# Kernel tuning notes

Hardware: AMD Instinct MI355X
Metric: run time of the kernel (lower is better)

Reference implementation:

```python
import jax, jax.numpy as jnp
import numpy as np

V, E, Hd, B, S = 50000, 256, 256, 128, 128  # vocab, embed, hidden, batch, seq


def setup_inputs() -> dict:
    key = jax.random.key(0)
    ks = jax.random.split(key, 16)
    std = 1.0 / np.sqrt(Hd)

    def u(k, shape, lim):
        return jax.random.uniform(k, shape, jnp.float32, -lim, lim)

    emb_table = jax.random.normal(ks[0], (V, E), jnp.float32)
    emb_table = emb_table.at[0].set(0.0)  # padding_idx=0

    inp = {
        'batch_size': B,
        'input_Q': jax.random.randint(ks[1], (S, B), 0, V),
        'input_C': jax.random.randint(ks[2], (S, B), 0, V),
        'input_C2': jax.random.randint(ks[3], (S, B), 0, V),
        'hidden_Q': jnp.zeros((2, B, Hd), jnp.float32),
        'cell_Q': jnp.zeros((2, B, Hd), jnp.float32),
        'hidden_C': jnp.zeros((2, B, Hd), jnp.float32),
        'cell_C': jnp.zeros((2, B, Hd), jnp.float32),
        'hidden_C2': jnp.zeros((2, B, Hd), jnp.float32),
        'cell_C2': jnp.zeros((2, B, Hd), jnp.float32),
        'emb_table': emb_table,
        'Wih_f': u(ks[4], (4 * Hd, E), std), 'Whh_f': u(ks[5], (4 * Hd, Hd), std),
        'bih_f': u(ks[6], (4 * Hd,), std), 'bhh_f': u(ks[7], (4 * Hd,), std),
        'Wih_b': u(ks[8], (4 * Hd, E), std), 'Whh_b': u(ks[9], (4 * Hd, Hd), std),
        'bih_b': u(ks[10], (4 * Hd,), std), 'bhh_b': u(ks[11], (4 * Hd,), std),
        'S1_W': u(ks[12], (2 * Hd, 2 * Hd), 0.1),  # init_weights: uniform(-0.1, 0.1)
        'S1_b': u(ks[13], (2 * Hd,), 1.0 / np.sqrt(2 * Hd)),
    }
    return inp


def _lstm_dir(xs, h0, c0, Wih, Whh, b):
    # xs: [S,B,E]; single direction LSTM, torch gate order i,f,g,o
    def step(carry, xt):
        h, c = carry
        g = xt @ Wih.T + h @ Whh.T + b  # [B,4H]
        i, f, gg, o = jnp.split(g, 4, axis=-1)
        c = jax.nn.sigmoid(f) * c + jax.nn.sigmoid(i) * jnp.tanh(gg)
        h = jax.nn.sigmoid(o) * jnp.tanh(c)
        return (h, c), h
    _, ys = jax.lax.scan(step, (h0, c0), xs)
    return ys  # [S,B,H]


def _bilstm(x, h0, c0, Wih_f, Whh_f, bih_f, bhh_f, Wih_b, Whh_b, bih_b, bhh_b):
    # x: [B,S,E] -> [B,S,2H]
    xs = jnp.swapaxes(x, 0, 1)
    yf = _lstm_dir(xs, h0[0], c0[0], Wih_f, Whh_f, bih_f + bhh_f)
    yb = _lstm_dir(xs[::-1], h0[1], c0[1], Wih_b, Whh_b, bih_b + bhh_b)[::-1]
    return jnp.swapaxes(jnp.concatenate([yf, yb], axis=-1), 0, 1)


def _attention(Q, C0, S1_W, S1_b):
    # Batched version of the per-sample loop: Q,C0 [B,S,2H]
    C = jnp.tanh(C0 @ S1_W.T + S1_b)                      # tanh(S1(C0))
    Hm = jnp.einsum('bsd,btd->bst', Q, C)                 # Q @ C.T
    AQ = jax.nn.softmax(Hm, axis=-1)                      # softmax over rows (torch dim=1 for 2D)
    AC = jax.nn.softmax(jnp.swapaxes(Hm, 1, 2), axis=-1)  # softmax(H.T)
    MQ = jnp.einsum('bst,btd->bsd', AQ, Q)
    MC = jnp.einsum('bst,btd->bsd', AC, MQ)
    b = Q.shape[0]
    return MQ.reshape(b, -1), MC.reshape(b, -1)


def reference(batch_size, input_Q, input_C, input_C2, hidden_Q, cell_Q,
              hidden_C, cell_C, hidden_C2, cell_C2, emb_table,
              Wih_f, Whh_f, bih_f, bhh_f, Wih_b, Whh_b, bih_b, bhh_b,
              S1_W, S1_b):
    lstm_w = (Wih_f, Whh_f, bih_f, bhh_f, Wih_b, Whh_b, bih_b, bhh_b)
    # forward() transposes [S,B] -> [B,S] before embedding
    q = emb_table[input_Q.T]
    c = emb_table[input_C.T]
    c2 = emb_table[input_C2.T]
    out_q = _bilstm(q, hidden_Q, cell_Q, *lstm_w)
    out_c = _bilstm(c, hidden_C, cell_C, *lstm_w)
    out_c2 = _bilstm(c2, hidden_C2, cell_C2, *lstm_w)
    attn_Q1, attn_C = _attention(out_q, out_c, S1_W, S1_b)
    attn_Q2, attn_C2 = _attention(out_q, out_c2, S1_W, S1_b)
    return (attn_Q1, attn_C, attn_Q2, attn_C2)
```

## Files before the change

kernel.cpp:

```cpp
#include <hip/hip_runtime.h>
#include <math.h>

namespace {

constexpr int S = 128;
constexpr int B = 128;
constexpr int E = 256;
constexpr int H = 256;

typedef unsigned short u16;
typedef __attribute__((ext_vector_type(8))) short short8v;
typedef __attribute__((ext_vector_type(4))) float f32x4;

__device__ __forceinline__ float sigmoidf(float x) { return 1.0f / (1.0f + expf(-x)); }
__device__ __forceinline__ u16 bf16rnd(float x) {
  unsigned u = __float_as_uint(x);
  return (u16)((u + 0x7FFFu + ((u >> 16) & 1u)) >> 16);
}
__device__ __forceinline__ float bf2f(u16 v) { return __uint_as_float(((unsigned)v) << 16); }
__device__ __forceinline__ void split2(float x, u16& h, u16& l) {
  h = bf16rnd(x);
  l = bf16rnd(x - bf2f(h));
}
__device__ __forceinline__ int gcol_of(int c) {
  return ((c >> 4) & 3) * 256 + ((c & 15) + ((c >> 6) << 4));
}


__global__ void split_pair(const float* __restrict__ src, u16* __restrict__ h,
                           u16* __restrict__ l, long n) {
  long i = (long)blockIdx.x * 256 + threadIdx.x;
  if (i < n) split2(src[i], h[i], l[i]);
}

__global__ void split_w_int(const float* __restrict__ W, u16* __restrict__ h,
                            u16* __restrict__ l) {
  int i = blockIdx.x * 256 + threadIdx.x;
  int c = i >> 8, k = i & 255;
  split2(W[gcol_of(c) * 256 + k], h[i], l[i]);
}

__global__ void make_bint(const float* __restrict__ bih, const float* __restrict__ bhh,
                          float* __restrict__ bint) {
  int c = blockIdx.x * 256 + threadIdx.x;
  int g = gcol_of(c);
  bint[c] = bih[g] + bhh[g];
}

__global__ void init_hc(const float* hQ, const float* cQ, const float* hC, const float* cC,
                        const float* hC2, const float* cC2,
                        u16* hH, u16* hL, float* cst) {
  int i = blockIdx.x * 256 + threadIdx.x;
  if (i >= 6 * B * H) return;
  int z = i / (B * H);
  int rem = i - z * (B * H);
  int input = z >> 1, dir = z & 1;
  const float* hs = input == 0 ? hQ : (input == 1 ? hC : hC2);
  const float* cs = input == 0 ? cQ : (input == 1 ? cC : cC2);
  split2(hs[dir * B * H + rem], hH[i], hL[i]);
  cst[i] = cs[dir * B * H + rem];
}

__global__ void zero_gen(int* gen) {
  if (threadIdx.x < 6) gen[threadIdx.x * 256] = 0;
}


#define MFMA_PROLOG                                        \
  const int tid = threadIdx.x;                             \
  const int wave = tid >> 6, lane = tid & 63;              \
  const int wr = wave >> 1, wc = wave & 1;                 \
  const int lrow = lane & 15, lk = lane >> 4;              \
  f32x4 acc[4][4];

#define MFMA_ZERO_ACC                                      \
  _Pragma("unroll") for (int a_ = 0; a_ < 4; ++a_)         \
  _Pragma("unroll") for (int b_ = 0; b_ < 4; ++b_)         \
      acc[a_][b_] = (f32x4){0.f, 0.f, 0.f, 0.f};

#define MFMA_INNER                                                             \
  __syncthreads();                                                             \
  short8v ah[4], al[4];                                                        \
  _Pragma("unroll") for (int mt = 0; mt < 4; ++mt) {                           \
    int r_ = wr * 64 + mt * 16 + lrow;                                         \
    ah[mt] = *(const short8v*)&Ah[r_ * 40 + lk * 8];                           \
    al[mt] = *(const short8v*)&Al[r_ * 40 + lk * 8];                           \
  }                                                                            \
  _Pragma("unroll") for (int nt = 0; nt < 4; ++nt) {                           \
    int c_ = wc * 64 + nt * 16 + lrow;                                         \
    short8v bh = *(const short8v*)&Bh[c_ * 40 + lk * 8];                       \
    short8v bl = *(const short8v*)&Bl[c_ * 40 + lk * 8];                       \
    _Pragma("unroll") for (int mt = 0; mt < 4; ++mt) {                         \
      acc[mt][nt] = __builtin_amdgcn_mfma_f32_16x16x32_bf16(ah[mt], bh, acc[mt][nt], 0, 0, 0); \
      acc[mt][nt] = __builtin_amdgcn_mfma_f32_16x16x32_bf16(ah[mt], bl, acc[mt][nt], 0, 0, 0); \
      acc[mt][nt] = __builtin_amdgcn_mfma_f32_16x16x32_bf16(al[mt], bh, acc[mt][nt], 0, 0, 0); \
    }                                                                          \
  }

__global__ __launch_bounds__(256) void proj_mfma(
    const int* __restrict__ idxQ, const int* __restrict__ idxC, const int* __restrict__ idxC2,
    const u16* __restrict__ embH, const u16* __restrict__ embL,
    const u16* __restrict__ wHf, const u16* __restrict__ wLf,
    const u16* __restrict__ wHb, const u16* __restrict__ wLb,
    const float* __restrict__ bintf, const float* __restrict__ bintb,
    float* __restrict__ gi, int phase)
{
  const int z = blockIdx.z, input = z >> 1, dir = z & 1;
  const int n0 = blockIdx.x * 128;
  const int tl = blockIdx.y;
  const int tb = (dir == 0) ? phase * 64 + tl : (64 - phase * 64) + tl;
  const int* idx = input == 0 ? idxQ : (input == 1 ? idxC : idxC2);
  const u16* wH = dir ? wHb : wHf;
  const u16* wL = dir ? wLb : wLf;
  const float* bint = dir ? bintb : bintf;

  __shared__ __align__(16) short Ah[128 * 40], Al[128 * 40], Bh[128 * 40], Bl[128 * 40];
  __shared__ int tok[128];
  MFMA_PROLOG
  if (tid < 128) tok[tid] = idx[tb * B + tid];
  MFMA_ZERO_ACC

  for (int kb = 0; kb < E; kb += 32) {
    __syncthreads();
#pragma unroll
    for (int i = 0; i < 2; ++i) {
      int e = i * 256 + tid;
      int r = e >> 2, kg = e & 3;
      long abase = (long)tok[r] * E + kb + kg * 8;
      *(short8v*)&Ah[r * 40 + kg * 8] = *(const short8v*)(embH + abase);
      *(short8v*)&Al[r * 40 + kg * 8] = *(const short8v*)(embL + abase);
      long bbase = (long)(n0 + r) * E + kb + kg * 8;
      *(short8v*)&Bh[r * 40 + kg * 8] = *(const short8v*)(wH + bbase);
      *(short8v*)&Bl[r * 40 + kg * 8] = *(const short8v*)(wL + bbase);
    }
    MFMA_INNER
  }

  float* gp = gi + ((long)z * 64 + tl) * 1024 * 128;
#pragma unroll
  for (int mt = 0; mt < 4; ++mt)
#pragma unroll
    for (int nt = 0; nt < 4; ++nt) {
      int c = n0 + wc * 64 + nt * 16 + lrow;
      float bv = bint[c];
      f32x4 v = acc[mt][nt];
      v.x += bv; v.y += bv; v.z += bv; v.w += bv;
      int rowb = wr * 64 + mt * 16 + lk * 4;
      *(f32x4*)&gp[(long)c * 128 + rowb] = v;
    }
}

__global__ __launch_bounds__(256) void lstm_persist(
    const u16* __restrict__ whHf, const u16* __restrict__ whLf,
    const u16* __restrict__ whHb, const u16* __restrict__ whLb,
    const float* __restrict__ gi,
    u16* __restrict__ hH, u16* __restrict__ hL, float* __restrict__ cst,
    u16* __restrict__ out3h, u16* __restrict__ out3l,
    int* __restrict__ gen, int phase)
{
  const int bx = blockIdx.x;
  const int z = bx >> 4, nb = bx & 15;
  const int input = z >> 1, dir = z & 1;
  const int n0c = nb * 64;
  const int tid = threadIdx.x;
  const int wave = tid >> 6, lane = tid & 63;
  const int lrow = lane & 15, lk = lane >> 4;
  const int wr = wave;
  const u16* wHp = dir ? whHb : whHf;
  const u16* wLp = dir ? whLb : whLf;

  __shared__ __align__(16) short WlH[64 * 264], WlL[64 * 264];

#pragma unroll
  for (int i = 0; i < 8; ++i) {
    int e = i * 256 + tid;
    int c = e >> 5, kc = e & 31;
    *(short8v*)&WlH[c * 264 + kc * 8] = *(const short8v*)(wHp + (long)(n0c + c) * 256 + kc * 8);
    *(short8v*)&WlL[c * 264 + kc * 8] = *(const short8v*)(wLp + (long)(n0c + c) * 256 + kc * 8);
  }
  __syncthreads();

  const long HS = (long)6 * B * H;
  const long zb = (long)z * B * H;
  const int u = nb * 16 + lrow;
  int* genz = gen + z * 256;
  u16* o3h = out3h + (long)input * B * S * 512;
  u16* o3l = out3l + (long)input * B * S * 512;

  for (int tl = 0; tl < 64; ++tl) {
    const int t_global = phase * 64 + tl;
    const int t_eff = dir ? (S - 1 - t_global) : t_global;
    const int local = (dir == 0) ? tl : 63 - tl;
    const int par = t_global & 1;

    f32x4 gv[2][4];
    {
      const float* gp = gi + ((long)z * 64 + local) * 1024 * 128;
#pragma unroll
      for (int mt = 0; mt < 2; ++mt)
#pragma unroll
        for (int nt = 0; nt < 4; ++nt) {
          int c = n0c + nt * 16 + lrow;
          int rowb = wr * 32 + mt * 16 + lk * 4;
          gv[mt][nt] = *(const f32x4*)&gp[(long)c * 128 + rowb];
        }
    }

    if (tl > 0) {
      if (tid == 0) {
        const int target = 16 * tl;
        while (__hip_atomic_load(genz, __ATOMIC_ACQUIRE, __HIP_MEMORY_SCOPE_AGENT) < target) {
          __builtin_amdgcn_s_sleep(2);
        }
      }
      __syncthreads();
    }

    const u16* hrH = hH + (long)par * HS + zb;
    const u16* hrL = hL + (long)par * HS + zb;

    f32x4 acc[2][4];
#pragma unroll
    for (int mt = 0; mt < 2; ++mt)
#pragma unroll
      for (int nt = 0; nt < 4; ++nt) acc[mt][nt] = gv[mt][nt];

#pragma unroll
    for (int kb = 0; kb < 8; ++kb) {
      short8v ah[2], al[2];
#pragma unroll
      for (int mt = 0; mt < 2; ++mt) {
        long ho = (long)(wr * 32 + mt * 16 + lrow) * 256 + kb * 32 + lk * 8;
        ah[mt] = *(const short8v*)(hrH + ho);
        al[mt] = *(const short8v*)(hrL + ho);
      }
#pragma unroll
      for (int nt = 0; nt < 4; ++nt) {
        int c = nt * 16 + lrow;
        short8v bh = *(const short8v*)&WlH[c * 264 + kb * 32 + lk * 8];
        short8v bl = *(const short8v*)&WlL[c * 264 + kb * 32 + lk * 8];
#pragma unroll
        for (int mt = 0; mt < 2; ++mt) {
          acc[mt][nt] = __builtin_amdgcn_mfma_f32_16x16x32_bf16(ah[mt], bh, acc[mt][nt], 0, 0, 0);
          acc[mt][nt] = __builtin_amdgcn_mfma_f32_16x16x32_bf16(ah[mt], bl, acc[mt][nt], 0, 0, 0);
          acc[mt][nt] = __builtin_amdgcn_mfma_f32_16x16x32_bf16(al[mt], bh, acc[mt][nt], 0, 0, 0);
        }
      }
    }

    float* cz = cst + zb;
    u16* hwH = hH + (long)(par ^ 1) * HS + zb;
    u16* hwL = hL + (long)(par ^ 1) * HS + zb;
#pragma unroll
    for (int mt = 0; mt < 2; ++mt)
#pragma unroll
      for (int rg = 0; rg < 4; ++rg) {
        int row = wr * 32 + mt * 16 + lk * 4 + rg;
        float ig = sigmoidf(acc[mt][0][rg]);
        float fg = sigmoidf(acc[mt][1][rg]);
        float gg = tanhf(acc[mt][2][rg]);
        float og = sigmoidf(acc[mt][3][rg]);
        long ci = (long)row * H + u;
        float cn = fg * cz[ci] + ig * gg;
        cz[ci] = cn;
        float hn = og * tanhf(cn);
        u16 hh, hl;
        split2(hn, hh, hl);
        hwH[ci] = hh;
        hwL[ci] = hl;
        long oi = ((long)row * S + t_eff) * 512 + dir * 256 + u;
        o3h[oi] = hh;
        o3l[oi] = hl;
      }

    asm volatile("s_waitcnt vmcnt(0)" ::: "memory");
    __syncthreads();
    if (tid == 0) {
      __hip_atomic_fetch_add(genz, 1, __ATOMIC_RELEASE, __HIP_MEMORY_SCOPE_AGENT);
    }
  }
}

__global__ __launch_bounds__(256) void ct_mfma(
    const u16* __restrict__ aH, const u16* __restrict__ aL,
    const u16* __restrict__ s1H, const u16* __restrict__ s1L,
    const float* __restrict__ s1b,
    u16* __restrict__ ctH, u16* __restrict__ ctL)
{
  const int n0 = blockIdx.x * 128, m0 = blockIdx.y * 128;
  __shared__ __align__(16) short Ah[128 * 40], Al[128 * 40], Bh[128 * 40], Bl[128 * 40];
  MFMA_PROLOG
  MFMA_ZERO_ACC

  for (int kb = 0; kb < 512; kb += 32) {
    __syncthreads();
#pragma unroll
    for (int i = 0; i < 2; ++i) {
      int e = i * 256 + tid;
      int r = e >> 2, kg = e & 3;
      long abase = (long)(m0 + r) * 512 + kb + kg * 8;
      *(short8v*)&Ah[r * 40 + kg * 8] = *(const short8v*)(aH + abase);
      *(short8v*)&Al[r * 40 + kg * 8] = *(const short8v*)(aL + abase);
      long bbase = (long)(n0 + r) * 512 + kb + kg * 8;
      *(short8v*)&Bh[r * 40 + kg * 8] = *(const short8v*)(s1H + bbase);
      *(short8v*)&Bl[r * 40 + kg * 8] = *(const short8v*)(s1L + bbase);
    }
    MFMA_INNER
  }

#pragma unroll
  for (int mt = 0; mt < 4; ++mt)
#pragma unroll
    for (int nt = 0; nt < 4; ++nt) {
      int c = n0 + wc * 64 + nt * 16 + lrow;
      float bv = s1b[c];
#pragma unroll
      for (int rg = 0; rg < 4; ++rg) {
        long m = m0 + wr * 64 + mt * 16 + lk * 4 + rg;
        u16 hh, ll;
        split2(tanhf(acc[mt][nt][rg] + bv), hh, ll);
        ctH[m * 512 + c] = hh;
        ctL[m * 512 + c] = ll;
      }
    }
}

__global__ __launch_bounds__(256) void hm_mfma(
    const u16* __restrict__ qH, const u16* __restrict__ qL,
    const u16* __restrict__ ctH, const u16* __restrict__ ctL,
    float* __restrict__ Hm)
{
  const int bb = blockIdx.x;
  const u16* aH = qH + (long)bb * S * 512;
  const u16* aL = qL + (long)bb * S * 512;
  const u16* bH = ctH + (long)bb * S * 512;
  const u16* bL = ctL + (long)bb * S * 512;
  __shared__ __align__(16) short Ah[128 * 40], Al[128 * 40], Bh[128 * 40], Bl[128 * 40];
  MFMA_PROLOG
  MFMA_ZERO_ACC

  for (int kb = 0; kb < 512; kb += 32) {
    __syncthreads();
#pragma unroll
    for (int i = 0; i < 2; ++i) {
      int e = i * 256 + tid;
      int r = e >> 2, kg = e & 3;
      long base = (long)r * 512 + kb + kg * 8;
      *(short8v*)&Ah[r * 40 + kg * 8] = *(const short8v*)(aH + base);
      *(short8v*)&Al[r * 40 + kg * 8] = *(const short8v*)(aL + base);
      *(short8v*)&Bh[r * 40 + kg * 8] = *(const short8v*)(bH + base);
      *(short8v*)&Bl[r * 40 + kg * 8] = *(const short8v*)(bL + base);
    }
    MFMA_INNER
  }

  float* out = Hm + (long)bb * S * S;
#pragma unroll
  for (int mt = 0; mt < 4; ++mt)
#pragma unroll
    for (int nt = 0; nt < 4; ++nt) {
      int c = wc * 64 + nt * 16 + lrow;
#pragma unroll
      for (int rg = 0; rg < 4; ++rg) {
        int m = wr * 64 + mt * 16 + lk * 4 + rg;
        out[(long)m * S + c] = acc[mt][nt][rg];
      }
    }
}

__global__ void transpose_qt(const u16* __restrict__ o3h, const u16* __restrict__ o3l,
                             u16* __restrict__ qth, u16* __restrict__ qtl) {
  const int b = blockIdx.z;
  const int c0 = blockIdx.x * 64, t0 = blockIdx.y * 64;
  __shared__ u16 tile[64][72];
  const int tid = threadIdx.x;
  for (int pl = 0; pl < 2; ++pl) {
    const u16* src = (pl ? o3l : o3h) + (long)b * S * 512;
    u16* dst = (pl ? qtl : qth) + (long)b * 512 * 128;
    __syncthreads();
#pragma unroll
    for (int i = 0; i < 2; ++i) {
      int e = i * 256 + tid;
      int r = e >> 3, sg = e & 7;
      *(short8v*)&tile[r][sg * 8] = *(const short8v*)(src + (long)(t0 + r) * 512 + c0 + sg * 8);
    }
    __syncthreads();
#pragma unroll
    for (int i = 0; i < 2; ++i) {
      int e = i * 256 + tid;
      int c = e >> 3, sg = e & 7;
      short8v v;
#pragma unroll
      for (int j = 0; j < 8; ++j) v[j] = tile[sg * 8 + j][c];
      *(short8v*)(dst + (long)(c0 + c) * 128 + t0 + sg * 8) = v;
    }
  }
}

template <bool WRITE_T>
__global__ __launch_bounds__(256) void pq_mfma(
    const u16* __restrict__ pH, const u16* __restrict__ pL,
    const u16* __restrict__ btH, const u16* __restrict__ btL,
    float* __restrict__ Cout, u16* __restrict__ tH, u16* __restrict__ tL)
{
  const int bb = blockIdx.z, n0 = blockIdx.x * 128;
  const u16* aHp = pH + (long)bb * 128 * 128;
  const u16* aLp = pL + (long)bb * 128 * 128;
  const u16* bHp = btH + ((long)bb * 512 + n0) * 128;
  const u16* bLp = btL + ((long)bb * 512 + n0) * 128;
  __shared__ __align__(16) short Ah[128 * 40], Al[128 * 40], Bh[128 * 40], Bl[128 * 40];
  MFMA_PROLOG
  MFMA_ZERO_ACC

  for (int kb = 0; kb < 128; kb += 32) {
    __syncthreads();
#pragma unroll
    for (int i = 0; i < 2; ++i) {
      int e = i * 256 + tid;
      int r = e >> 2, kg = e & 3;
      long base = (long)r * 128 + kb + kg * 8;
      *(short8v*)&Ah[r * 40 + kg * 8] = *(const short8v*)(aHp + base);
      *(short8v*)&Al[r * 40 + kg * 8] = *(const short8v*)(aLp + base);
      *(short8v*)&Bh[r * 40 + kg * 8] = *(const short8v*)(bHp + base);
      *(short8v*)&Bl[r * 40 + kg * 8] = *(const short8v*)(bLp + base);
    }
    MFMA_INNER
  }

  float* co = Cout + (long)bb * 128 * 512;
#pragma unroll
  for (int mt = 0; mt < 4; ++mt)
#pragma unroll
    for (int nt = 0; nt < 4; ++nt) {
      int c = n0 + wc * 64 + nt * 16 + lrow;
#pragma unroll
      for (int rg = 0; rg < 4; ++rg) {
        int m = wr * 64 + mt * 16 + lk * 4 + rg;
        float v = acc[mt][nt][rg];
        co[(long)m * 512 + c] = v;
        if (WRITE_T) {
          u16 hh, ll;
          split2(v, hh, ll);
          tH[((long)bb * 512 + c) * 128 + m] = hh;
          tL[((long)bb * 512 + c) * 128 + m] = ll;
        }
      }
    }
}

__global__ void softmax_row_bf(const float* __restrict__ Hm, u16* __restrict__ ph,
                               u16* __restrict__ pl) {
  const int row = blockIdx.x;
  const float* p = Hm + (long)row * S;
  const int l = threadIdx.x;
  float v0 = p[l], v1 = p[l + 64];
  float m = fmaxf(v0, v1);
#pragma unroll
  for (int o = 32; o > 0; o >>= 1) m = fmaxf(m, __shfl_xor(m, o));
  float e0 = expf(v0 - m), e1 = expf(v1 - m);
  float s = e0 + e1;
#pragma unroll
  for (int o = 32; o > 0; o >>= 1) s += __shfl_xor(s, o);
  float inv = 1.0f / s;
  u16 hh, ll;
  split2(e0 * inv, hh, ll);
  ph[(long)row * S + l] = hh; pl[(long)row * S + l] = ll;
  split2(e1 * inv, hh, ll);
  ph[(long)row * S + l + 64] = hh; pl[(long)row * S + l + 64] = ll;
}

__global__ void softmax_colT_bf(const float* __restrict__ Hm, u16* __restrict__ ph,
                                u16* __restrict__ pl) {
  const int b = blockIdx.x >> 7;
  const int col = blockIdx.x & 127;
  const float* p = Hm + (long)b * S * S + col;
  const int l = threadIdx.x;
  float v0 = p[(long)l * S], v1 = p[(long)(l + 64) * S];
  float m = fmaxf(v0, v1);
#pragma unroll
  for (int o = 32; o > 0; o >>= 1) m = fmaxf(m, __shfl_xor(m, o));
  float e0 = expf(v0 - m), e1 = expf(v1 - m);
  float s = e0 + e1;
#pragma unroll
  for (int o = 32; o > 0; o >>= 1) s += __shfl_xor(s, o);
  float inv = 1.0f / s;
  long q = ((long)b * S + col) * S;
  u16 hh, ll;
  split2(e0 * inv, hh, ll);
  ph[q + l] = hh; pl[q + l] = ll;
  split2(e1 * inv, hh, ll);
  ph[q + l + 64] = hh; pl[q + l + 64] = ll;
}

__global__ void softmax_row(const float* __restrict__ Hm, float* __restrict__ A) {
  const int row = blockIdx.x;
  const float* p = Hm + (long)row * S;
  const int l = threadIdx.x;
  float v0 = p[l], v1 = p[l + 64];
  float m = fmaxf(v0, v1);
#pragma unroll
  for (int o = 32; o > 0; o >>= 1) m = fmaxf(m, __shfl_xor(m, o));
  float e0 = expf(v0 - m), e1 = expf(v1 - m);
  float s = e0 + e1;
#pragma unroll
  for (int o = 32; o > 0; o >>= 1) s += __shfl_xor(s, o);
  float inv = 1.0f / s;
  float* q = A + (long)row * S;
  q[l] = e0 * inv; q[l + 64] = e1 * inv;
}

__global__ void softmax_colT(const float* __restrict__ Hm, float* __restrict__ A) {
  const int b = blockIdx.x >> 7;
  const int col = blockIdx.x & 127;
  const float* p = Hm + (long)b * S * S + col;
  const int l = threadIdx.x;
  float v0 = p[(long)l * S], v1 = p[(long)(l + 64) * S];
  float m = fmaxf(v0, v1);
#pragma unroll
  for (int o = 32; o > 0; o >>= 1) m = fmaxf(m, __shfl_xor(m, o));
  float e0 = expf(v0 - m), e1 = expf(v1 - m);
  float s = e0 + e1;
#pragma unroll
  for (int o = 32; o > 0; o >>= 1) s += __shfl_xor(s, o);
  float inv = 1.0f / s;
  float* q = A + ((long)b * S + col) * S;
  q[l] = e0 * inv; q[l + 64] = e1 * inv;
}


__global__ void init_state(const float* hQ, const float* cQ,
                           const float* hC, const float* cC,
                           const float* hC2, const float* cC2,
                           float* h0, float* c0) {
  int i = blockIdx.x * 256 + threadIdx.x;
  if (i >= 6 * B * H) return;
  int z = i / (B * H);
  int rem = i - z * (B * H);
  int input = z >> 1, dir = z & 1;
  const float* hs = input == 0 ? hQ : (input == 1 ? hC : hC2);
  const float* cs = input == 0 ? cQ : (input == 1 ? cC : cC2);
  h0[i] = hs[dir * B * H + rem];
  c0[i] = cs[dir * B * H + rem];
}

__global__ __launch_bounds__(256) void lstm_step(
    const int* __restrict__ idxQ, const int* __restrict__ idxC, const int* __restrict__ idxC2,
    const float* __restrict__ emb,
    const float* __restrict__ Wih_f, const float* __restrict__ Whh_f,
    const float* __restrict__ bih_f, const float* __restrict__ bhh_f,
    const float* __restrict__ Wih_b, const float* __restrict__ Whh_b,
    const float* __restrict__ bih_b, const float* __restrict__ bhh_b,
    const float* __restrict__ hread, float* __restrict__ hwrite,
    float* __restrict__ cstate, float* __restrict__ out3, int t)
{
  const int z = blockIdx.z;
  const int input = z >> 1, dir = z & 1;
  const int u0 = blockIdx.x * 16;
  const int b0 = blockIdx.y * 64;
  const int t_eff = dir ? (S - 1 - t) : t;
  const int* idx = input == 0 ? idxQ : (input == 1 ? idxC : idxC2);
  const float* Wih = dir ? Wih_b : Wih_f;
  const float* Whh = dir ? Whh_b : Whh_f;
  const float* bih = dir ? bih_b : bih_f;
  const float* bhh = dir ? bhh_b : bhh_f;

  __shared__ float Alds[64][68];
  __shared__ float Wl[64][68];
  __shared__ int tok[64];

  const int tid = threadIdx.x;
  if (tid < 64) tok[tid] = idx[t_eff * B + b0 + tid];

  const int uu = tid & 15;
  const int rg = tid >> 4;
  const int u = u0 + uu;

  float acc[4][4];
#pragma unroll
  for (int ri = 0; ri < 4; ++ri)
#pragma unroll
    for (int g = 0; g < 4; ++g)
      acc[ri][g] = bih[g * 256 + u] + bhh[g * 256 + u];

  for (int kc = 0; kc < 8; ++kc) {
    __syncthreads();
    if (kc < 4) {
      const int kb = kc * 64;
#pragma unroll
      for (int i = 0; i < 16; ++i) {
        int e = i * 256 + tid;
        int kk = e & 63, r = e >> 6;
        Alds[r][kk] = emb[(long)tok[r] * E + kb + kk];
      }
    } else {
      const int kb = (kc - 4) * 64;
      const float* hs = hread + ((long)z * B + b0) * H + kb;
#pragma unroll
      for (int i = 0; i < 16; ++i) {
        int e = i * 256 + tid;
        int kk = e & 63, r = e >> 6;
        Alds[r][kk] = hs[r * H + kk];
      }
    }
    {
      const float* Wsrc = (kc < 4) ? Wih : Whh;
      const int kb = (kc & 3) * 64;
#pragma unroll
      for (int i = 0; i < 16; ++i) {
        int e = i * 256 + tid;
        int kk = e & 63, c = e >> 6;
        int gcol = (c >> 4) * 256 + u0 + (c & 15);
        Wl[c][kk] = Wsrc[(long)gcol * H + kb + kk];
      }
    }
    __syncthreads();
#pragma unroll
    for (int k4 = 0; k4 < 64; k4 += 4) {
      float4 a[4], w[4];
#pragma unroll
      for (int ri = 0; ri < 4; ++ri) a[ri] = *(const float4*)&Alds[rg * 4 + ri][k4];
#pragma unroll
      for (int g = 0; g < 4; ++g) w[g] = *(const float4*)&Wl[g * 16 + uu][k4];
#pragma unroll
      for (int ri = 0; ri < 4; ++ri)
#pragma unroll
        for (int g = 0; g < 4; ++g)
          acc[ri][g] += a[ri].x * w[g].x + a[ri].y * w[g].y
                      + a[ri].z * w[g].z + a[ri].w * w[g].w;
    }
  }

  float* cs = cstate + (long)z * B * H;
  float* hw = hwrite + (long)z * B * H;
  float* op = out3 + (long)input * B * S * 2 * H;
#pragma unroll
  for (int ri = 0; ri < 4; ++ri) {
    int b = b0 + rg * 4 + ri;
    float ig = sigmoidf(acc[ri][0]);
    float fg = sigmoidf(acc[ri][1]);
    float gg = tanhf(acc[ri][2]);
    float og = sigmoidf(acc[ri][3]);
    float cn = fg * cs[b * H + u] + ig * gg;
    float hn = og * tanhf(cn);
    cs[b * H + u] = cn;
    hw[b * H + u] = hn;
    op[((long)b * S + t_eff) * (2 * H) + dir * H + u] = hn;
  }
}

template <bool TANH>
__global__ __launch_bounds__(256) void gemm_nt(
    const float* __restrict__ A, const float* __restrict__ B_,
    const float* __restrict__ bias, float* __restrict__ C,
    int lda, int ldb, int ldc, int K, long sA, long sB, long sC)
{
  A += blockIdx.z * sA; B_ += blockIdx.z * sB; C += blockIdx.z * sC;
  const int n0 = blockIdx.x * 64, m0 = blockIdx.y * 64;
  __shared__ float Alds[64][68], Blds[64][68];
  const int tid = threadIdx.x, uu = tid & 15, rg = tid >> 4;
  float acc[4][4] = {};
  for (int kb = 0; kb < K; kb += 64) {
    __syncthreads();
#pragma unroll
    for (int i = 0; i < 16; ++i) {
      int e = i * 256 + tid;
      int kk = e & 63, r = e >> 6;
      Alds[r][kk] = A[(long)(m0 + r) * lda + kb + kk];
      Blds[r][kk] = B_[(long)(n0 + r) * ldb + kb + kk];
    }
    __syncthreads();
#pragma unroll
    for (int k4 = 0; k4 < 64; k4 += 4) {
      float4 a[4], w[4];
#pragma unroll
      for (int ri = 0; ri < 4; ++ri) a[ri] = *(const float4*)&Alds[rg * 4 + ri][k4];
#pragma unroll
      for (int ci = 0; ci < 4; ++ci) w[ci] = *(const float4*)&Blds[ci * 16 + uu][k4];
#pragma unroll
      for (int ri = 0; ri < 4; ++ri)
#pragma unroll
        for (int ci = 0; ci < 4; ++ci)
          acc[ri][ci] += a[ri].x * w[ci].x + a[ri].y * w[ci].y
                       + a[ri].z * w[ci].z + a[ri].w * w[ci].w;
    }
  }
#pragma unroll
  for (int ri = 0; ri < 4; ++ri) {
    int m = m0 + rg * 4 + ri;
#pragma unroll
    for (int ci = 0; ci < 4; ++ci) {
      int n = n0 + ci * 16 + uu;
      float v = acc[ri][ci];
      if (bias) v += bias[n];
      if (TANH) v = tanhf(v);
      C[(long)m * ldc + n] = v;
    }
  }
}

__global__ __launch_bounds__(256) void gemm_nn(
    const float* __restrict__ A, const float* __restrict__ B_,
    float* __restrict__ C,
    int lda, int ldb, int ldc, int K, long sA, long sB, long sC)
{
  A += blockIdx.z * sA; B_ += blockIdx.z * sB; C += blockIdx.z * sC;
  const int n0 = blockIdx.x * 64, m0 = blockIdx.y * 64;
  __shared__ float Alds[64][68];
  __shared__ float Blds[64][68];
  const int tid = threadIdx.x, uu = tid & 15, rg = tid >> 4;
  float acc[4][4] = {};
  for (int kb = 0; kb < K; kb += 64) {
    __syncthreads();
#pragma unroll
    for (int i = 0; i < 16; ++i) {
      int e = i * 256 + tid;
      int kk = e & 63, r = e >> 6;
      Alds[r][kk] = A[(long)(m0 + r) * lda + kb + kk];
      Blds[r][kk] = B_[(long)(kb + r) * ldb + n0 + kk];
    }
    __syncthreads();
#pragma unroll
    for (int kk = 0; kk < 64; ++kk) {
      float4 w = *(const float4*)&Blds[kk][uu * 4];
      float a0 = Alds[rg * 4 + 0][kk], a1 = Alds[rg * 4 + 1][kk];
      float a2 = Alds[rg * 4 + 2][kk], a3 = Alds[rg * 4 + 3][kk];
      acc[0][0] += a0 * w.x; acc[0][1] += a0 * w.y; acc[0][2] += a0 * w.z; acc[0][3] += a0 * w.w;
      acc[1][0] += a1 * w.x; acc[1][1] += a1 * w.y; acc[1][2] += a1 * w.z; acc[1][3] += a1 * w.w;
      acc[2][0] += a2 * w.x; acc[2][1] += a2 * w.y; acc[2][2] += a2 * w.z; acc[2][3] += a2 * w.w;
      acc[3][0] += a3 * w.x; acc[3][1] += a3 * w.y; acc[3][2] += a3 * w.z; acc[3][3] += a3 * w.w;
    }
  }
#pragma unroll
  for (int ri = 0; ri < 4; ++ri) {
    int m = m0 + rg * 4 + ri;
    float4 v = make_float4(acc[ri][0], acc[ri][1], acc[ri][2], acc[ri][3]);
    *(float4*)&C[(long)m * ldc + n0 + uu * 4] = v;
  }
}

}

extern "C" void kernel_launch(void* const* d_in, const int* in_sizes, int n_in,
                              void* d_out, int out_size, void* d_ws, size_t ws_size,
                              hipStream_t stream) {
  const int* idxQ    = (const int*)d_in[1];
  const int* idxC    = (const int*)d_in[2];
  const int* idxC2   = (const int*)d_in[3];
  const float* hQ    = (const float*)d_in[4];
  const float* cQ    = (const float*)d_in[5];
  const float* hC    = (const float*)d_in[6];
  const float* cC    = (const float*)d_in[7];
  const float* hC2   = (const float*)d_in[8];
  const float* cC2   = (const float*)d_in[9];
  const float* emb   = (const float*)d_in[10];
  const float* Wih_f = (const float*)d_in[11];
  const float* Whh_f = (const float*)d_in[12];
  const float* bih_f = (const float*)d_in[13];
  const float* bhh_f = (const float*)d_in[14];
  const float* Wih_b = (const float*)d_in[15];
  const float* Whh_b = (const float*)d_in[16];
  const float* bih_b = (const float*)d_in[17];
  const float* bhh_b = (const float*)d_in[18];
  const float* S1W   = (const float*)d_in[19];
  const float* S1b   = (const float*)d_in[20];
  float* out = (float*)d_out;

  const long V = 50000;
  const long OUT1 = (long)B * S * 2 * H;

  size_t off = 0;
  auto alloc = [&](size_t bytes) { size_t o = off; off += (bytes + 255) & ~(size_t)255; return o; };
  const size_t o_gi   = alloc((size_t)6 * 64 * 1024 * 128 * 4);
  const size_t o_o3h  = alloc((size_t)3 * B * S * 512 * 2);
  const size_t o_o3l  = alloc((size_t)3 * B * S * 512 * 2);
  const size_t o_embH = alloc((size_t)V * E * 2);
  const size_t o_embL = alloc((size_t)V * E * 2);
  const size_t o_wihHf = alloc(1024 * 256 * 2), o_wihLf = alloc(1024 * 256 * 2);
  const size_t o_wihHb = alloc(1024 * 256 * 2), o_wihLb = alloc(1024 * 256 * 2);
  const size_t o_whhHf = alloc(1024 * 256 * 2), o_whhLf = alloc(1024 * 256 * 2);
  const size_t o_whhHb = alloc(1024 * 256 * 2), o_whhLb = alloc(1024 * 256 * 2);
  const size_t o_s1H  = alloc(512 * 512 * 2), o_s1L = alloc(512 * 512 * 2);
  const size_t o_bintf = alloc(1024 * 4), o_bintb = alloc(1024 * 4);
  const size_t o_hH   = alloc((size_t)2 * 6 * B * H * 2);
  const size_t o_hL   = alloc((size_t)2 * 6 * B * H * 2);
  const size_t o_cst  = alloc((size_t)6 * B * H * 4);
  const size_t o_gen  = alloc(6 * 256 * 4);
  const size_t need_fast = off;

  if (ws_size >= need_fast) {
    char* base = (char*)d_ws;
    float* gi = (float*)(base + o_gi);
    u16* o3h = (u16*)(base + o_o3h);
    u16* o3l = (u16*)(base + o_o3l);
    u16* embH = (u16*)(base + o_embH);
    u16* embL = (u16*)(base + o_embL);
    u16* wihHf = (u16*)(base + o_wihHf); u16* wihLf = (u16*)(base + o_wihLf);
    u16* wihHb = (u16*)(base + o_wihHb); u16* wihLb = (u16*)(base + o_wihLb);
    u16* whhHf = (u16*)(base + o_whhHf); u16* whhLf = (u16*)(base + o_whhLf);
    u16* whhHb = (u16*)(base + o_whhHb); u16* whhLb = (u16*)(base + o_whhLb);
    u16* s1H = (u16*)(base + o_s1H); u16* s1L = (u16*)(base + o_s1L);
    float* bintf = (float*)(base + o_bintf);
    float* bintb = (float*)(base + o_bintb);
    u16* hH = (u16*)(base + o_hH);
    u16* hL = (u16*)(base + o_hL);
    float* cst = (float*)(base + o_cst);
    int* gen = (int*)(base + o_gen);
    char* gib = base + o_gi;
    u16* ctH = (u16*)gib;
    u16* ctL = (u16*)(gib + 16777216);
    float* Hm = (float*)(gib + 2 * 16777216);
    u16* Ph  = (u16*)(gib + 2 * 16777216 + 8388608);
    u16* Pl  = (u16*)(gib + 2 * 16777216 + 8388608 + 4194304);
    u16* QtH = (u16*)(gib + 2 * 16777216 + 8388608 + 2 * 4194304);
    u16* QtL = (u16*)(gib + 3 * 16777216 + 8388608 + 2 * 4194304);
    u16* MQtH = (u16*)(gib + 4 * 16777216 + 8388608 + 2 * 4194304);
    u16* MQtL = (u16*)(gib + 5 * 16777216 + 8388608 + 2 * 4194304);

    split_pair<<<(int)((V * E + 255) / 256), 256, 0, stream>>>(emb, embH, embL, V * E);
    split_w_int<<<1024, 256, 0, stream>>>(Wih_f, wihHf, wihLf);
    split_w_int<<<1024, 256, 0, stream>>>(Wih_b, wihHb, wihLb);
    split_w_int<<<1024, 256, 0, stream>>>(Whh_f, whhHf, whhLf);
    split_w_int<<<1024, 256, 0, stream>>>(Whh_b, whhHb, whhLb);
    split_pair<<<1024, 256, 0, stream>>>(S1W, s1H, s1L, 512 * 512);
    make_bint<<<4, 256, 0, stream>>>(bih_f, bhh_f, bintf);
    make_bint<<<4, 256, 0, stream>>>(bih_b, bhh_b, bintb);
    init_hc<<<(6 * B * H + 255) / 256, 256, 0, stream>>>(hQ, cQ, hC, cC, hC2, cC2, hH, hL, cst);

    for (int phase = 0; phase < 2; ++phase) {
      proj_mfma<<<dim3(8, 64, 6), 256, 0, stream>>>(
          idxQ, idxC, idxC2, embH, embL,
          wihHf, wihLf, wihHb, wihLb, bintf, bintb, gi, phase);
      zero_gen<<<1, 64, 0, stream>>>(gen);
      {
        const u16* a0 = whhHf; const u16* a1 = whhLf;
        const u16* a2 = whhHb; const u16* a3 = whhLb;
        const float* a4 = gi; u16* a5 = hH; u16* a6 = hL;
        float* a7 = cst; u16* a8 = o3h; u16* a9 = o3l;
        int* a10 = gen; int a11 = phase;
        void* kargs[] = {(void*)&a0, (void*)&a1, (void*)&a2, (void*)&a3,
                         (void*)&a4, (void*)&a5, (void*)&a6, (void*)&a7,
                         (void*)&a8, (void*)&a9, (void*)&a10, (void*)&a11};
        hipLaunchCooperativeKernel((const void*)lstm_persist, dim3(96), dim3(256),
                                   kargs, 0, stream);
      }
    }

    transpose_qt<<<dim3(8, 2, 128), 256, 0, stream>>>(o3h, o3l, QtH, QtL);
    for (int p = 0; p < 2; ++p) {
      const u16* aH = o3h + (size_t)(1 + p) * B * S * 512;
      const u16* aL = o3l + (size_t)(1 + p) * B * S * 512;
      ct_mfma<<<dim3(4, 128), 256, 0, stream>>>(aH, aL, s1H, s1L, S1b, ctH, ctL);
      hm_mfma<<<128, 256, 0, stream>>>(o3h, o3l, ctH, ctL, Hm);
      softmax_row_bf<<<B * S, 64, 0, stream>>>(Hm, Ph, Pl);
      float* MQ = out + (long)(2 * p) * OUT1;
      pq_mfma<true><<<dim3(4, 1, 128), 256, 0, stream>>>(
          Ph, Pl, QtH, QtL, MQ, MQtH, MQtL);
      softmax_colT_bf<<<B * S, 64, 0, stream>>>(Hm, Ph, Pl);
      float* MC = out + (long)(2 * p + 1) * OUT1;
      pq_mfma<false><<<dim3(4, 1, 128), 256, 0, stream>>>(
          Ph, Pl, MQtH, MQtL, MC, nullptr, nullptr);
    }
    return;
  }

  const long ST = (long)6 * B * H;
  float* ws    = (float*)d_ws;
  float* out3  = ws;
  float* hbuf0 = out3 + 3 * OUT1;
  float* hbuf1 = hbuf0 + ST;
  float* cbuf  = hbuf1 + ST;
  float* Ct    = cbuf + ST;
  float* Hm    = Ct + OUT1;
  float* Ab    = Hm + (long)B * S * S;

  init_state<<<(6 * B * H + 255) / 256, 256, 0, stream>>>(hQ, cQ, hC, cC, hC2, cC2, hbuf0, cbuf);

  for (int t = 0; t < S; ++t) {
    float* hr = (t & 1) ? hbuf1 : hbuf0;
    float* hw = (t & 1) ? hbuf0 : hbuf1;
    lstm_step<<<dim3(16, 2, 6), 256, 0, stream>>>(
        idxQ, idxC, idxC2, emb,
        Wih_f, Whh_f, bih_f, bhh_f, Wih_b, Whh_b, bih_b, bhh_b,
        hr, hw, cbuf, out3, t);
  }

  for (int p = 0; p < 2; ++p) {
    const float* Q  = out3;
    const float* C0 = out3 + (long)(1 + p) * OUT1;
    gemm_nt<true><<<dim3(8, 256, 1), 256, 0, stream>>>(
        C0, S1W, S1b, Ct, 512, 512, 512, 512, 0, 0, 0);
    gemm_nt<false><<<dim3(2, 2, B), 256, 0, stream>>>(
        Q, Ct, nullptr, Hm, 512, 512, 128, 512,
        (long)S * 512, (long)S * 512, (long)S * S);
    softmax_row<<<B * S, 64, 0, stream>>>(Hm, Ab);
    float* MQ = out + (long)(2 * p) * OUT1;
    gemm_nn<<<dim3(8, 2, B), 256, 0, stream>>>(
        Ab, Q, MQ, 128, 512, 512, 128,
        (long)S * S, (long)S * 512, (long)S * 512);
    softmax_colT<<<B * S, 64, 0, stream>>>(Hm, Ab);
    float* MC = out + (long)(2 * p + 1) * OUT1;
    gemm_nn<<<dim3(8, 2, B), 256, 0, stream>>>(
        Ab, MQ, MC, 128, 512, 512, 128,
        (long)S * S, (long)S * 512, (long)S * 512);
  }
}
```

Measured before the change: 2.498 ms.

## Fuse input projection into persistent LSTM kernel and keep cell state in registers

Removes the separate proj_mfma input-projection GEMM and its large gi buffer. Each persistent block now keeps both W_ih and W_hh slices in LDS, gathers embedding rows per timestep and computes the input projection before waiting on the generation barrier, so that work overlaps the wait for other blocks' h. The cell state is held in registers instead of global memory, and the two phases become one cooperative launch of 128 blocks (96 active). The cost is doubled LDS per block and gather loads from the embedding table on the recurrent critical path.

```diff
diff --git a/kernel.cpp b/kernel.cpp
--- a/kernel.cpp
+++ b/kernel.cpp
@@ -97,148 +97,102 @@
     }                                                                          \
   }
 
-__global__ __launch_bounds__(256) void proj_mfma(
+__global__ __launch_bounds__(256) void lstm_fused(
     const int* __restrict__ idxQ, const int* __restrict__ idxC, const int* __restrict__ idxC2,
     const u16* __restrict__ embH, const u16* __restrict__ embL,
-    const u16* __restrict__ wHf, const u16* __restrict__ wLf,
-    const u16* __restrict__ wHb, const u16* __restrict__ wLb,
+    const u16* __restrict__ wihHf, const u16* __restrict__ wihLf,
+    const u16* __restrict__ wihHb, const u16* __restrict__ wihLb,
+    const u16* __restrict__ whhHf, const u16* __restrict__ whhLf,
+    const u16* __restrict__ whhHb, const u16* __restrict__ whhLb,
     const float* __restrict__ bintf, const float* __restrict__ bintb,
-    float* __restrict__ gi, int phase)
-{
-  const int z = blockIdx.z, input = z >> 1, dir = z & 1;
-  const int n0 = blockIdx.x * 128;
-  const int tl = blockIdx.y;
-  const int tb = (dir == 0) ? phase * 64 + tl : (64 - phase * 64) + tl;
-  const int* idx = input == 0 ? idxQ : (input == 1 ? idxC : idxC2);
-  const u16* wH = dir ? wHb : wHf;
-  const u16* wL = dir ? wLb : wLf;
-  const float* bint = dir ? bintb : bintf;
-
-  __shared__ __align__(16) short Ah[128 * 40], Al[128 * 40], Bh[128 * 40], Bl[128 * 40];
-  __shared__ int tok[128];
-  MFMA_PROLOG
-  if (tid < 128) tok[tid] = idx[tb * B + tid];
-  MFMA_ZERO_ACC
-
-  for (int kb = 0; kb < E; kb += 32) {
-    __syncthreads();
-#pragma unroll
-    for (int i = 0; i < 2; ++i) {
-      int e = i * 256 + tid;
-      int r = e >> 2, kg = e & 3;
-      long abase = (long)tok[r] * E + kb + kg * 8;
-      *(short8v*)&Ah[r * 40 + kg * 8] = *(const short8v*)(embH + abase);
-      *(short8v*)&Al[r * 40 + kg * 8] = *(const short8v*)(embL + abase);
-      long bbase = (long)(n0 + r) * E + kb + kg * 8;
-      *(short8v*)&Bh[r * 40 + kg * 8] = *(const short8v*)(wH + bbase);
-      *(short8v*)&Bl[r * 40 + kg * 8] = *(const short8v*)(wL + bbase);
-    }
-    MFMA_INNER
-  }
-
-  float* gp = gi + ((long)z * 64 + tl) * 1024 * 128;
-#pragma unroll
-  for (int mt = 0; mt < 4; ++mt)
-#pragma unroll
-    for (int nt = 0; nt < 4; ++nt) {
-      int c = n0 + wc * 64 + nt * 16 + lrow;
-      float bv = bint[c];
-      f32x4 v = acc[mt][nt];
-      v.x += bv; v.y += bv; v.z += bv; v.w += bv;
-      int rowb = wr * 64 + mt * 16 + lk * 4;
-      *(f32x4*)&gp[(long)c * 128 + rowb] = v;
-    }
-}
-
-__global__ __launch_bounds__(256) void lstm_persist(
-    const u16* __restrict__ whHf, const u16* __restrict__ whLf,
-    const u16* __restrict__ whHb, const u16* __restrict__ whLb,
-    const float* __restrict__ gi,
-    u16* __restrict__ hH, u16* __restrict__ hL, float* __restrict__ cst,
+    u16* __restrict__ hH, u16* __restrict__ hL, const float* __restrict__ cst0,
     u16* __restrict__ out3h, u16* __restrict__ out3l,
-    int* __restrict__ gen, int phase)
+    int* __restrict__ gen)
 {
   const int bx = blockIdx.x;
-  const int z = bx >> 4, nb = bx & 15;
+  const int z = bx & 7;
+  if (z >= 6) return;
+  const int nb = bx >> 3;
   const int input = z >> 1, dir = z & 1;
   const int n0c = nb * 64;
   const int tid = threadIdx.x;
   const int wave = tid >> 6, lane = tid & 63;
   const int lrow = lane & 15, lk = lane >> 4;
   const int wr = wave;
-  const u16* wHp = dir ? whHb : whHf;
-  const u16* wLp = dir ? whLb : whLf;
-
-  __shared__ __align__(16) short WlH[64 * 264], WlL[64 * 264];
+  const int* idx = input == 0 ? idxQ : (input == 1 ? idxC : idxC2);
+  const u16* wiHp = dir ? wihHb : wihHf;
+  const u16* wiLp = dir ? wihLb : wihLf;
+  const u16* whHp = dir ? whhHb : whhHf;
+  const u16* whLp = dir ? whhLb : whhLf;
+  const float* bint = dir ? bintb : bintf;
+
+  __shared__ __align__(16) short WiH[64 * 264], WiL[64 * 264];
+  __shared__ __align__(16) short WhH[64 * 264], WhL[64 * 264];
+  __shared__ int tok[128];
 
 #pragma unroll
   for (int i = 0; i < 8; ++i) {
     int e = i * 256 + tid;
     int c = e >> 5, kc = e & 31;
-    *(short8v*)&WlH[c * 264 + kc * 8] = *(const short8v*)(wHp + (long)(n0c + c) * 256 + kc * 8);
-    *(short8v*)&WlL[c * 264 + kc * 8] = *(const short8v*)(wLp + (long)(n0c + c) * 256 + kc * 8);
-  }
-  __syncthreads();
+    long src = (long)(n0c + c) * 256 + kc * 8;
+    *(short8v*)&WiH[c * 264 + kc * 8] = *(const short8v*)(wiHp + src);
+    *(short8v*)&WiL[c * 264 + kc * 8] = *(const short8v*)(wiLp + src);
+    *(short8v*)&WhH[c * 264 + kc * 8] = *(const short8v*)(whHp + src);
+    *(short8v*)&WhL[c * 264 + kc * 8] = *(const short8v*)(whLp + src);
+  }
+
+  const int u = nb * 16 + lrow;
+  float bintv[4];
+#pragma unroll
+  for (int nt = 0; nt < 4; ++nt) bintv[nt] = bint[n0c + nt * 16 + lrow];
 
   const long HS = (long)6 * B * H;
   const long zb = (long)z * B * H;
-  const int u = nb * 16 + lrow;
+  float creg[2][4];
+#pragma unroll
+  for (int mt = 0; mt < 2; ++mt)
+#pragma unroll
+    for (int rg = 0; rg < 4; ++rg)
+      creg[mt][rg] = cst0[zb + (long)(wr * 32 + mt * 16 + lk * 4 + rg) * H + u];
+
   int* genz = gen + z * 256;
   u16* o3h = out3h + (long)input * B * S * 512;
   u16* o3l = out3l + (long)input * B * S * 512;
 
-  for (int tl = 0; tl < 64; ++tl) {
-    const int t_global = phase * 64 + tl;
-    const int t_eff = dir ? (S - 1 - t_global) : t_global;
-    const int local = (dir == 0) ? tl : 63 - tl;
-    const int par = t_global & 1;
-
-    f32x4 gv[2][4];
-    {
-      const float* gp = gi + ((long)z * 64 + local) * 1024 * 128;
-#pragma unroll
-      for (int mt = 0; mt < 2; ++mt)
-#pragma unroll
-        for (int nt = 0; nt < 4; ++nt) {
-          int c = n0c + nt * 16 + lrow;
-          int rowb = wr * 32 + mt * 16 + lk * 4;
-          gv[mt][nt] = *(const f32x4*)&gp[(long)c * 128 + rowb];
-        }
-    }
-
-    if (tl > 0) {
-      if (tid == 0) {
-        const int target = 16 * tl;
-        while (__hip_atomic_load(genz, __ATOMIC_ACQUIRE, __HIP_MEMORY_SCOPE_AGENT) < target) {
-          __builtin_amdgcn_s_sleep(2);
-        }
-      }
-      __syncthreads();
-    }
-
-    const u16* hrH = hH + (long)par * HS + zb;
-    const u16* hrL = hL + (long)par * HS + zb;
+  __syncthreads();
+
+  for (int t = 0; t < S; ++t) {
+    const int t_eff = dir ? (S - 1 - t) : t;
+    const int par = t & 1;
+
+    if (tid < 128) tok[tid] = idx[t_eff * B + tid];
+    __syncthreads();
+    const int tv0 = tok[wr * 32 + lrow];
+    const int tv1 = tok[wr * 32 + 16 + lrow];
 
     f32x4 acc[2][4];
 #pragma unroll
     for (int mt = 0; mt < 2; ++mt)
 #pragma unroll
-      for (int nt = 0; nt < 4; ++nt) acc[mt][nt] = gv[mt][nt];
+      for (int nt = 0; nt < 4; ++nt)
+        acc[mt][nt] = (f32x4){bintv[nt], bintv[nt], bintv[nt], bintv[nt]};
 
 #pragma unroll
     for (int kb = 0; kb < 8; ++kb) {
       short8v ah[2], al[2];
-#pragma unroll
-      for (int mt = 0; mt < 2; ++mt) {
-        long ho = (long)(wr * 32 + mt * 16 + lrow) * 256 + kb * 32 + lk * 8;
-        ah[mt] = *(const short8v*)(hrH + ho);
-        al[mt] = *(const short8v*)(hrL + ho);
+      {
+        long e0 = (long)tv0 * 256 + kb * 32 + lk * 8;
+        long e1 = (long)tv1 * 256 + kb * 32 + lk * 8;
+        ah[0] = *(const short8v*)(embH + e0);
+        al[0] = *(const short8v*)(embL + e0);
+        ah[1] = *(const short8v*)(embH + e1);
+        al[1] = *(const short8v*)(embL + e1);
       }
 #pragma unroll
       for (int nt = 0; nt < 4; ++nt) {
         int c = nt * 16 + lrow;
-        short8v bh = *(const short8v*)&WlH[c * 264 + kb * 32 + lk * 8];
-        short8v bl = *(const short8v*)&WlL[c * 264 + kb * 32 + lk * 8];
+        short8v bh = *(const short8v*)&WiH[c * 264 + kb * 32 + lk * 8];
+        short8v bl = *(const short8v*)&WiL[c * 264 + kb * 32 + lk * 8];
 #pragma unroll
         for (int mt = 0; mt < 2; ++mt) {
           acc[mt][nt] = __builtin_amdgcn_mfma_f32_16x16x32_bf16(ah[mt], bh, acc[mt][nt], 0, 0, 0);
@@ -248,7 +202,41 @@
       }
     }
 
-    float* cz = cst + zb;
+    if (t > 0) {
+      if (tid == 0) {
+        const int target = 16 * t;
+        while (__hip_atomic_load(genz, __ATOMIC_ACQUIRE, __HIP_MEMORY_SCOPE_AGENT) < target) {
+          __builtin_amdgcn_s_sleep(2);
+        }
+      }
+      __syncthreads();
+    }
+
+    const u16* hrH = hH + (long)par * HS + zb;
+    const u16* hrL = hL + (long)par * HS + zb;
+#pragma unroll
+    for (int kb = 0; kb < 8; ++kb) {
+      short8v ah[2], al[2];
+#pragma unroll
+      for (int mt = 0; mt < 2; ++mt) {
+        long ho = (long)(wr * 32 + mt * 16 + lrow) * 256 + kb * 32 + lk * 8;
+        ah[mt] = *(const short8v*)(hrH + ho);
+        al[mt] = *(const short8v*)(hrL + ho);
+      }
+#pragma unroll
+      for (int nt = 0; nt < 4; ++nt) {
+        int c = nt * 16 + lrow;
+        short8v bh = *(const short8v*)&WhH[c * 264 + kb * 32 + lk * 8];
+        short8v bl = *(const short8v*)&WhL[c * 264 + kb * 32 + lk * 8];
+#pragma unroll
+        for (int mt = 0; mt < 2; ++mt) {
+          acc[mt][nt] = __builtin_amdgcn_mfma_f32_16x16x32_bf16(ah[mt], bh, acc[mt][nt], 0, 0, 0);
+          acc[mt][nt] = __builtin_amdgcn_mfma_f32_16x16x32_bf16(ah[mt], bl, acc[mt][nt], 0, 0, 0);
+          acc[mt][nt] = __builtin_amdgcn_mfma_f32_16x16x32_bf16(al[mt], bh, acc[mt][nt], 0, 0, 0);
+        }
+      }
+    }
+
     u16* hwH = hH + (long)(par ^ 1) * HS + zb;
     u16* hwL = hL + (long)(par ^ 1) * HS + zb;
 #pragma unroll
@@ -260,12 +248,12 @@
         float fg = sigmoidf(acc[mt][1][rg]);
         float gg = tanhf(acc[mt][2][rg]);
         float og = sigmoidf(acc[mt][3][rg]);
-        long ci = (long)row * H + u;
-        float cn = fg * cz[ci] + ig * gg;
-        cz[ci] = cn;
+        float cn = fg * creg[mt][rg] + ig * gg;
+        creg[mt][rg] = cn;
         float hn = og * tanhf(cn);
         u16 hh, hl;
         split2(hn, hh, hl);
+        long ci = (long)row * H + u;
         hwH[ci] = hh;
         hwL[ci] = hl;
         long oi = ((long)row * S + t_eff) * 512 + dir * 256 + u;
@@ -770,7 +758,6 @@
 
   size_t off = 0;
   auto alloc = [&](size_t bytes) { size_t o = off; off += (bytes + 255) & ~(size_t)255; return o; };
-  const size_t o_gi   = alloc((size_t)6 * 64 * 1024 * 128 * 4);
   const size_t o_o3h  = alloc((size_t)3 * B * S * 512 * 2);
   const size_t o_o3l  = alloc((size_t)3 * B * S * 512 * 2);
   const size_t o_embH = alloc((size_t)V * E * 2);
@@ -785,11 +772,19 @@
   const size_t o_hL   = alloc((size_t)2 * 6 * B * H * 2);
   const size_t o_cst  = alloc((size_t)6 * B * H * 4);
   const size_t o_gen  = alloc(6 * 256 * 4);
+  const size_t o_ctH  = alloc((size_t)B * S * 512 * 2);
+  const size_t o_ctL  = alloc((size_t)B * S * 512 * 2);
+  const size_t o_Hm   = alloc((size_t)B * S * S * 4);
+  const size_t o_Ph   = alloc((size_t)B * S * S * 2);
+  const size_t o_Pl   = alloc((size_t)B * S * S * 2);
+  const size_t o_QtH  = alloc((size_t)B * 512 * 128 * 2);
+  const size_t o_QtL  = alloc((size_t)B * 512 * 128 * 2);
+  const size_t o_MQtH = alloc((size_t)B * 512 * 128 * 2);
+  const size_t o_MQtL = alloc((size_t)B * 512 * 128 * 2);
   const size_t need_fast = off;
 
   if (ws_size >= need_fast) {
     char* base = (char*)d_ws;
-    float* gi = (float*)(base + o_gi);
     u16* o3h = (u16*)(base + o_o3h);
     u16* o3l = (u16*)(base + o_o3l);
     u16* embH = (u16*)(base + o_embH);
@@ -805,16 +800,15 @@
     u16* hL = (u16*)(base + o_hL);
     float* cst = (float*)(base + o_cst);
     int* gen = (int*)(base + o_gen);
-    char* gib = base + o_gi;
-    u16* ctH = (u16*)gib;
-    u16* ctL = (u16*)(gib + 16777216);
-    float* Hm = (float*)(gib + 2 * 16777216);
-    u16* Ph  = (u16*)(gib + 2 * 16777216 + 8388608);
-    u16* Pl  = (u16*)(gib + 2 * 16777216 + 8388608 + 4194304);
-    u16* QtH = (u16*)(gib + 2 * 16777216 + 8388608 + 2 * 4194304);
-    u16* QtL = (u16*)(gib + 3 * 16777216 + 8388608 + 2 * 4194304);
-    u16* MQtH = (u16*)(gib + 4 * 16777216 + 8388608 + 2 * 4194304);
-    u16* MQtL = (u16*)(gib + 5 * 16777216 + 8388608 + 2 * 4194304);
+    u16* ctH = (u16*)(base + o_ctH);
+    u16* ctL = (u16*)(base + o_ctL);
+    float* Hm = (float*)(base + o_Hm);
+    u16* Ph = (u16*)(base + o_Ph);
+    u16* Pl = (u16*)(base + o_Pl);
+    u16* QtH = (u16*)(base + o_QtH);
+    u16* QtL = (u16*)(base + o_QtL);
+    u16* MQtH = (u16*)(base + o_MQtH);
+    u16* MQtL = (u16*)(base + o_MQtL);
 
     split_pair<<<(int)((V * E + 255) / 256), 256, 0, stream>>>(emb, embH, embL, V * E);
     split_w_int<<<1024, 256, 0, stream>>>(Wih_f, wihHf, wihLf);
@@ -825,24 +819,25 @@
     make_bint<<<4, 256, 0, stream>>>(bih_f, bhh_f, bintf);
     make_bint<<<4, 256, 0, stream>>>(bih_b, bhh_b, bintb);
     init_hc<<<(6 * B * H + 255) / 256, 256, 0, stream>>>(hQ, cQ, hC, cC, hC2, cC2, hH, hL, cst);
-
-    for (int phase = 0; phase < 2; ++phase) {
-      proj_mfma<<<dim3(8, 64, 6), 256, 0, stream>>>(
-          idxQ, idxC, idxC2, embH, embL,
-          wihHf, wihLf, wihHb, wihLb, bintf, bintb, gi, phase);
-      zero_gen<<<1, 64, 0, stream>>>(gen);
-      {
-        const u16* a0 = whhHf; const u16* a1 = whhLf;
-        const u16* a2 = whhHb; const u16* a3 = whhLb;
-        const float* a4 = gi; u16* a5 = hH; u16* a6 = hL;
-        float* a7 = cst; u16* a8 = o3h; u16* a9 = o3l;
-        int* a10 = gen; int a11 = phase;
-        void* kargs[] = {(void*)&a0, (void*)&a1, (void*)&a2, (void*)&a3,
-                         (void*)&a4, (void*)&a5, (void*)&a6, (void*)&a7,
-                         (void*)&a8, (void*)&a9, (void*)&a10, (void*)&a11};
-        hipLaunchCooperativeKernel((const void*)lstm_persist, dim3(96), dim3(256),
-                                   kargs, 0, stream);
-      }
+    zero_gen<<<1, 64, 0, stream>>>(gen);
+
+    {
+      const int* a0 = idxQ; const int* a1 = idxC; const int* a2 = idxC2;
+      const u16* a3 = embH; const u16* a4 = embL;
+      const u16* a5 = wihHf; const u16* a6 = wihLf;
+      const u16* a7 = wihHb; const u16* a8 = wihLb;
+      const u16* a9 = whhHf; const u16* a10 = whhLf;
+      const u16* a11 = whhHb; const u16* a12 = whhLb;
+      const float* a13 = bintf; const float* a14 = bintb;
+      u16* a15 = hH; u16* a16 = hL; const float* a17 = cst;
+      u16* a18 = o3h; u16* a19 = o3l; int* a20 = gen;
+      void* kargs[] = {(void*)&a0, (void*)&a1, (void*)&a2, (void*)&a3, (void*)&a4,
+                       (void*)&a5, (void*)&a6, (void*)&a7, (void*)&a8, (void*)&a9,
+                       (void*)&a10, (void*)&a11, (void*)&a12, (void*)&a13, (void*)&a14,
+                       (void*)&a15, (void*)&a16, (void*)&a17, (void*)&a18, (void*)&a19,
+                       (void*)&a20};
+      hipLaunchCooperativeKernel((const void*)lstm_fused, dim3(128), dim3(256),
+                                 kargs, 0, stream);
     }
 
     transpose_qt<<<dim3(8, 2, 128), 256, 0, stream>>>(o3h, o3l, QtH, QtL);
```

Result: faster. 2.240 ms (-10.3%).
